# Kernel optimization log

Hardware: AMD Instinct MI355X
Metric: run time of the kernel (lower is better)

## Reference

```python
import jax, jax.numpy as jnp
import numpy as np

B, C, H, W = 16, 256, 64, 64
HEADS = 4  # kvl produces (heads-1)=3 groups: lfeat, k, v


def setup_inputs() -> dict:
    key = jax.random.key(0)
    ks = jax.random.split(key, 8)
    s = 0.02
    return {
        "x": jax.random.normal(ks[0], (B, C, H, W), jnp.float32),
        "q_input": jax.random.normal(ks[1], (B, C, H, W), jnp.float32),
        "w_kvl": jax.random.normal(ks[2], (C * (HEADS - 1), C), jnp.float32) * s,
        "b_kvl": jnp.zeros((C * (HEADS - 1),), jnp.float32),
        "w_q": jax.random.normal(ks[3], (C, C), jnp.float32) * s,
        "b_q": jnp.zeros((C,), jnp.float32),
        "w_proj": jax.random.normal(ks[4], (C, 2 * C), jnp.float32) * s,
        "b_proj": jnp.zeros((C,), jnp.float32),
    }


def gelu(x):
    return jax.nn.gelu(x, approximate=False)  # torch nn.GELU default (erf)


def reference(x, q_input, w_kvl, b_kvl, w_q, b_q, w_proj, b_proj):
    b, c, h, w = x.shape
    n = h * w
    # 1x1 conv kvl: C -> 3C, then GELU
    kvl = gelu(jnp.einsum('oc,bchw->bohw', w_kvl, x) + b_kvl[None, :, None, None])
    kvl = kvl.reshape(b, HEADS - 1, c, h, w)
    lfeat = kvl[:, 0]                      # [B,C,H,W]
    k = kvl[:, 1].reshape(b, c, n)          # [B,C,HW]
    v = kvl[:, 2].reshape(b, c, n)          # [B,C,HW]
    # 1x1 conv q: C -> C
    q = jnp.einsum('oc,bchw->bohw', w_q, q_input) + b_q[None, :, None, None]
    q = q.reshape(b, c, n)                  # [B,C,HW]
    # channel-wise attention: qk is [B,C,C] (no scaling, per source)
    qk = jnp.einsum('bcn,bdn->bcd', q, k)
    qk = jax.nn.softmax(qk, axis=-1)
    x2 = jnp.einsum('bcd,bdn->bcn', qk, v).reshape(b, c, h, w)
    cat = jnp.concatenate([lfeat, x2], axis=1)  # [B,2C,H,W]
    out = jnp.einsum('oc,bchw->bohw', w_proj, cat) + b_proj[None, :, None, None]
    return gelu(out)
```

## Files before the change

### kernel.cpp

```cpp
#include <hip/hip_runtime.h>
#include <hip/hip_bf16.h>
#include <hip/hip_fp16.h>

typedef _Float16 f16;
typedef _Float16 half8 __attribute__((ext_vector_type(8)));
typedef _Float16 half4 __attribute__((ext_vector_type(4)));
typedef float f32x4 __attribute__((ext_vector_type(4)));

__device__ __forceinline__ float gelu_f(float x) {
  return 0.5f * x * (1.0f + erff(x * 0.70710678118654752f));
}

__device__ __forceinline__ void gll16(const void* g, void* l) {
  __builtin_amdgcn_global_load_lds((const __attribute__((address_space(1))) void*)g,
                                   (__attribute__((address_space(3))) void*)l,
                                   16, 0, 0);
}

template<int KK, bool OUT_F16>
__global__ __launch_bounds__(512, 2)
void gemm_wstat(const f16* __restrict__ W, size_t sW,
                const f16* __restrict__ Act, size_t sA,
                void* __restrict__ Dv, size_t sD,
                const float* __restrict__ bias,
                int panelsPerBlock, int blocksPerBatch)
{
  constexpr int PN  = (KK == 512) ? 32 : 64;
  constexpr int PB  = PN * KK * 2;
  constexpr int NKS = KK / 32;
  constexpr int NT  = PN / 16;
  __shared__ __align__(16) char lds[2 * PB];

  const int t = threadIdx.x;
  const int l = t & 63;
  const int w = t >> 6;
  const int bid = blockIdx.x;
  const int b = bid / blocksPerBatch;
  const int blkInB = bid - b * blocksPerBatch;

  const f16* Wb = W + (size_t)b * sW;
  const f16* Ab = Act + (size_t)b * sA;

  half8 wf[2][NKS];
#pragma unroll
  for (int mt = 0; mt < 2; ++mt)
#pragma unroll
    for (int ks = 0; ks < NKS; ++ks) {
      const int row = w * 32 + mt * 16 + (l & 15);
      wf[mt][ks] = *(const half8*)(Wb + (size_t)row * KK + ks * 32 + (l >> 4) * 8);
    }

  auto stage = [&](int buf, int p) {
    const int n0 = (blkInB * panelsPerBlock + p) * PN;
#pragma unroll
    for (int i = 0; i < 4; ++i) {
      const int off = (i * 8 + w) * 1024 + l * 16;
      const int row = off / (KK * 2);
      const int chunk = (off & (KK * 2 - 1)) >> 4;
      const int lch = chunk ^ (row & 7);
      gll16(Ab + (size_t)(n0 + row) * KK + lch * 8, lds + buf * PB + (i * 8 + w) * 1024);
    }
  };

  int buf = 0;
  stage(0, 0);
  for (int p = 0; p < panelsPerBlock; ++p) {
    if (p + 1 < panelsPerBlock) {
      stage(buf ^ 1, p + 1);
      asm volatile("s_waitcnt vmcnt(4)" ::: "memory");
    } else {
      asm volatile("s_waitcnt vmcnt(0)" ::: "memory");
    }
    asm volatile("s_barrier" ::: "memory");

    f32x4 acc[2][NT];
#pragma unroll
    for (int mt = 0; mt < 2; ++mt)
#pragma unroll
      for (int nt = 0; nt < NT; ++nt)
        acc[mt][nt] = (f32x4){0.f, 0.f, 0.f, 0.f};
#pragma unroll
    for (int ks = 0; ks < NKS; ++ks) {
      half8 bf[NT];
#pragma unroll
      for (int nt = 0; nt < NT; ++nt) {
        const int row = nt * 16 + (l & 15);
        const int ch = (ks * 4 + (l >> 4)) ^ (row & 7);
        bf[nt] = *(const half8*)(lds + buf * PB + row * (KK * 2) + ch * 16);
      }
#pragma unroll
      for (int mt = 0; mt < 2; ++mt)
#pragma unroll
        for (int nt = 0; nt < NT; ++nt)
          acc[mt][nt] = __builtin_amdgcn_mfma_f32_16x16x32_f16(wf[mt][ks], bf[nt], acc[mt][nt], 0, 0, 0);
    }

    const int n0 = (blkInB * panelsPerBlock + p) * PN;
#pragma unroll
    for (int mt = 0; mt < 2; ++mt) {
      const int rb = w * 32 + mt * 16 + ((l >> 4) << 2);
#pragma unroll
      for (int nt = 0; nt < NT; ++nt) {
        const int col = n0 + nt * 16 + (l & 15);
#pragma unroll
        for (int j = 0; j < 4; ++j) {
          const int rr = rb + j;
          float v = gelu_f(acc[mt][nt][j] + bias[rr]);
          if (OUT_F16) ((f16*)Dv + (size_t)b * sD)[(size_t)rr * 4096 + col] = (f16)v;
          else         ((float*)Dv + (size_t)b * sD)[(size_t)rr * 4096 + col] = v;
        }
      }
    }
    asm volatile("s_barrier" ::: "memory");
    buf ^= 1;
  }
}

__global__ __launch_bounds__(512, 2)
void gemm_sstat(const f16* __restrict__ Act, size_t sA,
                const f16* __restrict__ W,
                f16* __restrict__ Dp, size_t sD,
                const float* __restrict__ bias,
                int panelsPerBlock, int blocksPerBatch)
{
  constexpr int KK = 256, PN = 64, PB = PN * KK * 2;
  __shared__ __align__(16) char lds[2 * PB];

  const int t = threadIdx.x;
  const int l = t & 63;
  const int w = t >> 6;
  const int bid = blockIdx.x;
  const int b = bid / blocksPerBatch;
  const int blkInB = bid - b * blocksPerBatch;

  const f16* Ab = Act + (size_t)b * sA;

  half8 wf[4][8];
#pragma unroll
  for (int ct = 0; ct < 4; ++ct)
#pragma unroll
    for (int ks = 0; ks < 8; ++ks) {
      const int row = w * 64 + ct * 16 + (l & 15);
      wf[ct][ks] = *(const half8*)(W + (size_t)row * 256 + ks * 32 + (l >> 4) * 8);
    }

  auto stage = [&](int buf, int p) {
    const int n0 = (blkInB * panelsPerBlock + p) * PN;
#pragma unroll
    for (int i = 0; i < 4; ++i) {
      const int off = (i * 8 + w) * 1024 + l * 16;
      const int row = off >> 9;
      const int chunk = (off & 511) >> 4;
      const int lch = chunk ^ (row & 7);
      gll16(Ab + (size_t)(n0 + row) * 256 + lch * 8, lds + buf * PB + (i * 8 + w) * 1024);
    }
  };

  int buf = 0;
  stage(0, 0);
  for (int p = 0; p < panelsPerBlock; ++p) {
    if (p + 1 < panelsPerBlock) {
      stage(buf ^ 1, p + 1);
      asm volatile("s_waitcnt vmcnt(4)" ::: "memory");
    } else {
      asm volatile("s_waitcnt vmcnt(0)" ::: "memory");
    }
    asm volatile("s_barrier" ::: "memory");

    f32x4 acc[4][4];
#pragma unroll
    for (int nt = 0; nt < 4; ++nt)
#pragma unroll
      for (int ct = 0; ct < 4; ++ct)
        acc[nt][ct] = (f32x4){0.f, 0.f, 0.f, 0.f};
#pragma unroll
    for (int ks = 0; ks < 8; ++ks) {
      half8 af[4];
#pragma unroll
      for (int nt = 0; nt < 4; ++nt) {
        const int row = nt * 16 + (l & 15);
        const int ch = (ks * 4 + (l >> 4)) ^ (row & 7);
        af[nt] = *(const half8*)(lds + buf * PB + row * 512 + ch * 16);
      }
#pragma unroll
      for (int nt = 0; nt < 4; ++nt)
#pragma unroll
        for (int ct = 0; ct < 4; ++ct)
          acc[nt][ct] = __builtin_amdgcn_mfma_f32_16x16x32_f16(af[nt], wf[ct][ks], acc[nt][ct], 0, 0, 0);
    }

    const int n0 = (blkInB * panelsPerBlock + p) * PN;
    f16* Db = Dp + (size_t)b * sD;
#pragma unroll
    for (int nt = 0; nt < 4; ++nt) {
      const int rb = n0 + nt * 16 + ((l >> 4) << 2);
#pragma unroll
      for (int ct = 0; ct < 4; ++ct) {
        const int col = w * 64 + ct * 16 + (l & 15);
        const int bi = col + (col >= 256 ? 256 : 0);
        const float bv = bias[bi];
#pragma unroll
        for (int j = 0; j < 4; ++j)
          Db[(size_t)(rb + j) * 512 + col] = (f16)gelu_f(acc[nt][ct][j] + bv);
      }
    }
    asm volatile("s_barrier" ::: "memory");
    buf ^= 1;
  }
}

#define BM 128
#define BN 128
#define BK 32
template<int BIAS, bool GELU_ACT, bool OUT_F16, bool KSPLIT>
__global__ __launch_bounds__(256)
void gemm_tn(const f16* __restrict__ P, size_t sP, int ldP,
             const f16* __restrict__ Q, size_t sQ, int ldQ,
             void* __restrict__ Dv, size_t sD, int ldD,
             const float* __restrict__ bias, const float* __restrict__ bias2,
             int M, int N, int K, int nks)
{
  __shared__ __align__(16) f16 ldsA[BM * BK];
  __shared__ __align__(16) f16 ldsB[BM * BK];

  const int t = threadIdx.x;
  const int l = t & 63;
  const int wid = t >> 6;
  const int wr = wid >> 1;
  const int wc = wid & 1;

  const int z = blockIdx.z;
  const int b = z / nks;
  const int s = z - b * nks;
  const int kLen = K / nks;
  const int k0 = s * kLen;

  const int mBase = blockIdx.y * BM;
  const int nBase = blockIdx.x * BN;

  const f16* Pb = P + (size_t)b * sP;
  const f16* Qb = Q + (size_t)b * sQ;

  f32x4 acc[4][4];
#pragma unroll
  for (int i = 0; i < 4; ++i)
#pragma unroll
    for (int j = 0; j < 4; ++j)
      acc[i][j] = (f32x4){0.f, 0.f, 0.f, 0.f};

  const int nk = kLen / BK;
  for (int kt = 0; kt < nk; ++kt) {
    const int kk = k0 + kt * BK;
#pragma unroll
    for (int c = 0; c < 2; ++c) {
      const int off = c * 4096 + wid * 1024 + l * 16;
      const int row = off >> 6;
      const int gch = ((off >> 4) & 3) ^ ((row >> 1) & 3);
      gll16(Pb + (size_t)(mBase + row) * ldP + kk + gch * 8,
            (char*)ldsA + c * 4096 + wid * 1024);
      gll16(Qb + (size_t)(nBase + row) * ldQ + kk + gch * 8,
            (char*)ldsB + c * 4096 + wid * 1024);
    }
    asm volatile("s_waitcnt vmcnt(0)" ::: "memory");
    __syncthreads();

    half8 af[4], bf[4];
#pragma unroll
    for (int mi = 0; mi < 4; ++mi) {
      const int row = wr * 64 + mi * 16 + (l & 15);
      const int phys = row * 64 + ((((l >> 4) ^ (row >> 1)) & 3) << 4);
      af[mi] = *(const half8*)((const char*)ldsA + phys);
    }
#pragma unroll
    for (int ni = 0; ni < 4; ++ni) {
      const int row = wc * 64 + ni * 16 + (l & 15);
      const int phys = row * 64 + ((((l >> 4) ^ (row >> 1)) & 3) << 4);
      bf[ni] = *(const half8*)((const char*)ldsB + phys);
    }
#pragma unroll
    for (int mi = 0; mi < 4; ++mi)
#pragma unroll
      for (int ni = 0; ni < 4; ++ni)
        acc[mi][ni] = __builtin_amdgcn_mfma_f32_16x16x32_f16(af[mi], bf[ni], acc[mi][ni], 0, 0, 0);
    __syncthreads();
  }

  float* Dsplit = nullptr; f16* D16 = nullptr; float* D32 = nullptr;
  if (KSPLIT)       Dsplit = (float*)Dv + (size_t)z * (size_t)(M * N);
  else if (OUT_F16) D16    = (f16*)Dv + (size_t)b * sD;
  else              D32    = (float*)Dv + (size_t)b * sD;

#pragma unroll
  for (int mi = 0; mi < 4; ++mi) {
    const int rb = mBase + wr * 64 + mi * 16 + ((l >> 4) << 2);
#pragma unroll
    for (int ni = 0; ni < 4; ++ni) {
      const int col = nBase + wc * 64 + ni * 16 + (l & 15);
#pragma unroll
      for (int j = 0; j < 4; ++j) {
        float v = acc[mi][ni][j];
        const int rr = rb + j;
        if (BIAS == 1) v += bias[rr];
        if (BIAS == 2) v += bias[col];
        if (BIAS == 3) v += bias[rr] * bias2[(size_t)b * N + col];
        if (GELU_ACT) v = gelu_f(v);
        if (KSPLIT)       Dsplit[(size_t)rr * ldD + col] = v;
        else if (OUT_F16) D16[(size_t)rr * ldD + col] = (f16)v;
        else              D32[(size_t)rr * ldD + col] = v;
      }
    }
  }
}

__global__ __launch_bounds__(256)
void transpose64(const float* __restrict__ in, f16* __restrict__ outp) {
  __shared__ float tile[64][65];
  const int b = blockIdx.z, c0 = blockIdx.y * 64, n0 = blockIdx.x * 64;
  const int t = threadIdx.x;
  const float* ib = in + (size_t)b * 1048576;
  f16* ob = outp + (size_t)b * 1048576;
  const int cl = t >> 4, c4 = t & 15;
#pragma unroll
  for (int i = 0; i < 4; ++i) {
    float4 v = *(const float4*)(ib + (size_t)(c0 + cl + i * 16) * 4096 + n0 + c4 * 4);
    tile[cl + i * 16][c4 * 4 + 0] = v.x;
    tile[cl + i * 16][c4 * 4 + 1] = v.y;
    tile[cl + i * 16][c4 * 4 + 2] = v.z;
    tile[cl + i * 16][c4 * 4 + 3] = v.w;
  }
  __syncthreads();
  const int nl = t >> 3, ch = t & 7;
#pragma unroll
  for (int i = 0; i < 2; ++i) {
    const int n = nl + i * 32;
    half8 h;
#pragma unroll
    for (int e = 0; e < 8; ++e) h[e] = (f16)tile[ch * 8 + e][n];
    *(half8*)(ob + (size_t)(n0 + n) * 256 + c0 + ch * 8) = h;
  }
}

__global__ __launch_bounds__(256)
void cvtf16(const float* __restrict__ in, f16* __restrict__ outp, int n8) {
  int i = blockIdx.x * 256 + threadIdx.x;
  if (i < n8) {
    float4 a = ((const float4*)in)[2 * i];
    float4 c = ((const float4*)in)[2 * i + 1];
    half8 h = {(f16)a.x, (f16)a.y, (f16)a.z, (f16)a.w,
               (f16)c.x, (f16)c.y, (f16)c.z, (f16)c.w};
    ((half8*)outp)[i] = h;
  }
}

__global__ __launch_bounds__(256)
void wsplit(const float* __restrict__ wp, f16* __restrict__ Wx, f16* __restrict__ Wcat) {
  const int o = blockIdx.x, c = threadIdx.x;
  const f16 lf = (f16)wp[o * 512 + c];
  Wx[o * 256 + c] = (f16)wp[o * 512 + 256 + c];
#pragma unroll
  for (int b = 0; b < 16; ++b) Wcat[(size_t)b * 131072 + o * 512 + c] = lf;
}

__global__ __launch_bounds__(256)
void ksum_k(const f16* __restrict__ kH, float* __restrict__ ks) {
  const int r = blockIdx.x * 4 + (threadIdx.x >> 6);
  const int l = threadIdx.x & 63;
  const half8* row = (const half8*)(kH + (size_t)r * 4096);
  float s = 0.f;
#pragma unroll
  for (int j = 0; j < 8; ++j) {
    half8 h = row[l + 64 * j];
#pragma unroll
    for (int e = 0; e < 8; ++e) s += (float)h[e];
  }
#pragma unroll
  for (int off = 32; off; off >>= 1) s += __shfl_xor(s, off);
  if (l == 0) ks[r] = s;
}

__global__ __launch_bounds__(256)
void reduce8_k(const float* __restrict__ part, f16* __restrict__ m1T) {
  const int i = blockIdx.x * 256 + threadIdx.x;
  const int b = i >> 14;
  const int e4 = i & 16383;
  const float4* base = (const float4*)part + (size_t)b * 131072 + e4;
  float4 s = {0.f, 0.f, 0.f, 0.f};
#pragma unroll
  for (int zz = 0; zz < 8; ++zz) {
    float4 p = base[(size_t)zz * 16384];
    s.x += p.x; s.y += p.y; s.z += p.z; s.w += p.w;
  }
  half4 h = {(f16)s.x, (f16)s.y, (f16)s.z, (f16)s.w};
  ((half4*)m1T)[i] = h;
}

__global__ __launch_bounds__(256)
void softmaxT(const float* __restrict__ qk, f16* __restrict__ pT) {
  __shared__ f16 sm[4][256];
  const int wid = threadIdx.x >> 6, l = threadIdx.x & 63;
  const int b = blockIdx.y;
  const int c = blockIdx.x * 4 + wid;
  const float* row = qk + ((size_t)b * 256 + c) * 256;
  float v[4];
#pragma unroll
  for (int j = 0; j < 4; ++j) v[j] = row[l + 64 * j];
  float m = fmaxf(fmaxf(v[0], v[1]), fmaxf(v[2], v[3]));
#pragma unroll
  for (int off = 32; off; off >>= 1) m = fmaxf(m, __shfl_xor(m, off));
  float e[4], sum = 0.f;
#pragma unroll
  for (int j = 0; j < 4; ++j) { e[j] = expf(v[j] - m); sum += e[j]; }
#pragma unroll
  for (int off = 32; off; off >>= 1) sum += __shfl_xor(sum, off);
  const float inv = 1.0f / sum;
#pragma unroll
  for (int j = 0; j < 4; ++j) sm[wid][l + 64 * j] = (f16)(e[j] * inv);
  __syncthreads();
  const int d = threadIdx.x;
  half4 h = {sm[0][d], sm[1][d], sm[2][d], sm[3][d]};
  *(half4*)(pT + ((size_t)b * 256 + d) * 256 + blockIdx.x * 4) = h;
}

extern "C" void kernel_launch(void* const* d_in, const int* in_sizes, int n_in,
                              void* d_out, int out_size, void* d_ws, size_t ws_size,
                              hipStream_t stream) {
  const float* x      = (const float*)d_in[0];
  const float* qin    = (const float*)d_in[1];
  const float* w_kvl  = (const float*)d_in[2];
  const float* b_kvl  = (const float*)d_in[3];
  const float* w_q    = (const float*)d_in[4];
  const float* b_q    = (const float*)d_in[5];
  const float* w_proj = (const float*)d_in[6];
  const float* b_proj = (const float*)d_in[7];
  float* out = (float*)d_out;
  char* ws = (char*)d_ws;

  if (ws_size < 182000000) return;

  f16*   xt    = (f16*)(ws + 0);
  float* part  = (float*)(ws + 0);
  f16*   qin16 = (f16*)(ws + 33554432);
  f16*   kH    = (f16*)(ws + 67108864);
  f16*   lvT   = (f16*)(ws + 100663296);
  f16*   wk_lv = (f16*)(ws + 167772160);
  f16*   wkK   = (f16*)(ws + 168034304);
  f16*   wq16  = (f16*)(ws + 168165376);
  f16*   Wx16  = (f16*)(ws + 168296448);
  f16*   Wcat  = (f16*)(ws + 168427520);
  float* ksum  = (float*)(ws + 172621824);
  f16*   m1T   = (f16*)(ws + 172638208);
  float* qkb   = (float*)(ws + 174735360);
  f16*   pT    = (f16*)(ws + 178929664);

  const size_t sAct = 1048576;
  dim3 blk(256), blk512(512);

  transpose64<<<dim3(64, 4, 16), blk, 0, stream>>>(x, xt);
  cvtf16<<<dim3(8192), blk, 0, stream>>>(qin, qin16, 2097152);
  cvtf16<<<dim3(32), blk, 0, stream>>>(w_kvl, wk_lv, 8192);
  cvtf16<<<dim3(32), blk, 0, stream>>>(w_kvl + 131072, wk_lv + 65536, 8192);
  cvtf16<<<dim3(32), blk, 0, stream>>>(w_kvl + 65536, wkK, 8192);
  cvtf16<<<dim3(32), blk, 0, stream>>>(w_q, wq16, 8192);
  wsplit<<<dim3(256), blk, 0, stream>>>(w_proj, Wx16, Wcat);

  hipLaunchKernelGGL((gemm_wstat<256, true>), dim3(512), blk512, 0, stream,
      wkK, (size_t)0, xt, sAct, (void*)kH, sAct, b_kvl + 256, 2, 32);
  gemm_sstat<<<dim3(512), blk512, 0, stream>>>(xt, sAct, wk_lv, lvT, (size_t)2097152, b_kvl, 2, 32);

  ksum_k<<<dim3(1024), blk, 0, stream>>>(kH, ksum);

  hipLaunchKernelGGL((gemm_tn<0, false, false, true>), dim3(2, 2, 128), blk, 0, stream,
      kH, sAct, 4096, qin16, sAct, 4096,
      (void*)part, (size_t)0, 256, (const float*)nullptr, (const float*)nullptr, 256, 256, 4096, 8);
  reduce8_k<<<dim3(1024), blk, 0, stream>>>(part, m1T);

  hipLaunchKernelGGL((gemm_tn<3, false, false, false>), dim3(2, 2, 16), blk, 0, stream,
      wq16, (size_t)0, 256, m1T, (size_t)65536, 256,
      (void*)qkb, (size_t)65536, 256, b_q, ksum, 256, 256, 256, 1);

  softmaxT<<<dim3(64, 16), blk, 0, stream>>>(qkb, pT);

  hipLaunchKernelGGL((gemm_tn<0, false, true, false>), dim3(2, 2, 16), blk, 0, stream,
      Wx16, (size_t)0, 256, pT, (size_t)65536, 256,
      (void*)(Wcat + 256), (size_t)131072, 512, (const float*)nullptr, (const float*)nullptr, 256, 256, 256, 1);

  hipLaunchKernelGGL((gemm_wstat<512, false>), dim3(512), blk512, 0, stream,
      Wcat, (size_t)131072, lvT, (size_t)2097152, (void*)out, sAct, b_proj, 4, 32);
}
```

Measured before the change: 383.9 us.

## Stage GEMM epilogues through LDS for coalesced stores; double-buffer gemm_tn loads

The weight-stationary and activation-stationary GEMMs now write their GELU outputs into the just-consumed LDS panel with a swizzled layout, then read them back as 16-byte vectors for coalesced global stores, replacing scattered 2- or 4-byte stores. Bias loads in gemm_sstat move out of the panel loop. The wait counts are adjusted for the extra outstanding stores. gemm_tn gains a double-buffered LDS prefetch with precomputed source pointers, so the next K tile loads while the current one computes. This adds barriers and LDS traffic per panel and is sensitive to whether the vmcnt values correctly count the pending loads and stores.

```diff
diff --git a/kernel.cpp b/kernel.cpp
--- a/kernel.cpp
+++ b/kernel.cpp
@@ -67,7 +67,8 @@
   for (int p = 0; p < panelsPerBlock; ++p) {
     if (p + 1 < panelsPerBlock) {
       stage(buf ^ 1, p + 1);
-      asm volatile("s_waitcnt vmcnt(4)" ::: "memory");
+      if (p == 0) asm volatile("s_waitcnt vmcnt(4)" ::: "memory");
+      else        asm volatile("s_waitcnt vmcnt(8)" ::: "memory");
     } else {
       asm volatile("s_waitcnt vmcnt(0)" ::: "memory");
     }
@@ -94,21 +95,43 @@
         for (int nt = 0; nt < NT; ++nt)
           acc[mt][nt] = __builtin_amdgcn_mfma_f32_16x16x32_f16(wf[mt][ks], bf[nt], acc[mt][nt], 0, 0, 0);
     }
+    asm volatile("s_barrier" ::: "memory");
 
     const int n0 = (blkInB * panelsPerBlock + p) * PN;
 #pragma unroll
     for (int mt = 0; mt < 2; ++mt) {
-      const int rb = w * 32 + mt * 16 + ((l >> 4) << 2);
+      const int mbase = w * 32 + mt * 16 + ((l >> 4) << 2);
 #pragma unroll
       for (int nt = 0; nt < NT; ++nt) {
-        const int col = n0 + nt * 16 + (l & 15);
+        const int ncol = nt * 16 + (l & 15);
 #pragma unroll
         for (int j = 0; j < 4; ++j) {
-          const int rr = rb + j;
-          float v = gelu_f(acc[mt][nt][j] + bias[rr]);
-          if (OUT_F16) ((f16*)Dv + (size_t)b * sD)[(size_t)rr * 4096 + col] = (f16)v;
-          else         ((float*)Dv + (size_t)b * sD)[(size_t)rr * 4096 + col] = v;
+          const int mrow = mbase + j;
+          float v = gelu_f(acc[mt][nt][j] + bias[mrow]);
+          if (OUT_F16) {
+            const int phys = mrow * 128 + ((ncol * 2) ^ ((mrow & 7) << 4));
+            *(f16*)(lds + buf * PB + phys) = (f16)v;
+          } else {
+            const int phys = mrow * 128 + ((ncol * 4) ^ ((mrow & 7) << 4));
+            *(float*)(lds + buf * PB + phys) = v;
+          }
         }
+      }
+    }
+    asm volatile("s_waitcnt lgkmcnt(0)" ::: "memory");
+    asm volatile("s_barrier" ::: "memory");
+#pragma unroll
+    for (int st = 0; st < 4; ++st) {
+      const int i = st * 8192 + t * 16;
+      const int mrow = i >> 7;
+      const int cb = i & 127;
+      const int phys = mrow * 128 + (cb ^ ((mrow & 7) << 4));
+      if (OUT_F16) {
+        half8 hv = *(const half8*)(lds + buf * PB + phys);
+        *(half8*)((char*)Dv + ((size_t)b * sD + (size_t)mrow * 4096 + n0) * 2 + cb) = hv;
+      } else {
+        float4 fv = *(const float4*)(lds + buf * PB + phys);
+        *(float4*)((char*)Dv + ((size_t)b * sD + (size_t)mrow * 4096 + n0) * 4 + cb) = fv;
       }
     }
     asm volatile("s_barrier" ::: "memory");
@@ -134,6 +157,7 @@
   const int blkInB = bid - b * blocksPerBatch;
 
   const f16* Ab = Act + (size_t)b * sA;
+  f16* Db = Dp + (size_t)b * sD;
 
   half8 wf[4][8];
 #pragma unroll
@@ -143,6 +167,13 @@
       const int row = w * 64 + ct * 16 + (l & 15);
       wf[ct][ks] = *(const half8*)(W + (size_t)row * 256 + ks * 32 + (l >> 4) * 8);
     }
+
+  float bv[4];
+#pragma unroll
+  for (int ct = 0; ct < 4; ++ct) {
+    const int col = w * 64 + ct * 16 + (l & 15);
+    bv[ct] = bias[col + (col >= 256 ? 256 : 0)];
+  }
 
   auto stage = [&](int buf, int p) {
     const int n0 = (blkInB * panelsPerBlock + p) * PN;
@@ -188,23 +219,39 @@
         for (int ct = 0; ct < 4; ++ct)
           acc[nt][ct] = __builtin_amdgcn_mfma_f32_16x16x32_f16(af[nt], wf[ct][ks], acc[nt][ct], 0, 0, 0);
     }
+    asm volatile("s_barrier" ::: "memory");
 
     const int n0 = (blkInB * panelsPerBlock + p) * PN;
-    f16* Db = Dp + (size_t)b * sD;
-#pragma unroll
-    for (int nt = 0; nt < 4; ++nt) {
-      const int rb = n0 + nt * 16 + ((l >> 4) << 2);
-#pragma unroll
-      for (int ct = 0; ct < 4; ++ct) {
-        const int col = w * 64 + ct * 16 + (l & 15);
-        const int bi = col + (col >= 256 ? 256 : 0);
-        const float bv = bias[bi];
-#pragma unroll
-        for (int j = 0; j < 4; ++j)
-          Db[(size_t)(rb + j) * 512 + col] = (f16)gelu_f(acc[nt][ct][j] + bv);
-      }
-    }
-    asm volatile("s_barrier" ::: "memory");
+#pragma unroll
+    for (int h = 0; h < 2; ++h) {
+#pragma unroll
+      for (int nt2 = 0; nt2 < 2; ++nt2) {
+        const int nt = h * 2 + nt2;
+        const int rbase = nt2 * 16 + ((l >> 4) << 2);
+#pragma unroll
+        for (int ct = 0; ct < 4; ++ct) {
+          const int colb = (w * 64 + ct * 16 + (l & 15)) * 2;
+#pragma unroll
+          for (int j = 0; j < 4; ++j) {
+            const int row = rbase + j;
+            const int phys = row * 1024 + (colb ^ (((row >> 2) & 3) << 5));
+            *(f16*)(lds + buf * PB + phys) = (f16)gelu_f(acc[nt][ct][j] + bv[ct]);
+          }
+        }
+      }
+      asm volatile("s_waitcnt lgkmcnt(0)" ::: "memory");
+      asm volatile("s_barrier" ::: "memory");
+#pragma unroll
+      for (int st = 0; st < 4; ++st) {
+        const int i = st * 8192 + t * 16;
+        const int row = i >> 10;
+        const int cb = i & 1023;
+        const int phys = row * 1024 + (cb ^ (((row >> 2) & 3) << 5));
+        half8 hv = *(const half8*)(lds + buf * PB + phys);
+        *(half8*)((char*)Db + ((size_t)(n0 + h * 32 + row) * 512) * 2 + cb) = hv;
+      }
+      asm volatile("s_barrier" ::: "memory");
+    }
     buf ^= 1;
   }
 }
@@ -220,8 +267,7 @@
              const float* __restrict__ bias, const float* __restrict__ bias2,
              int M, int N, int K, int nks)
 {
-  __shared__ __align__(16) f16 ldsA[BM * BK];
-  __shared__ __align__(16) f16 ldsB[BM * BK];
+  __shared__ __align__(16) char lds[32768];
 
   const int t = threadIdx.x;
   const int l = t & 63;
@@ -241,6 +287,29 @@
   const f16* Pb = P + (size_t)b * sP;
   const f16* Qb = Q + (size_t)b * sQ;
 
+  const f16* srcA[2];
+  const f16* srcB[2];
+  int dstOff[2];
+#pragma unroll
+  for (int c = 0; c < 2; ++c) {
+    const int off = c * 4096 + wid * 1024 + l * 16;
+    const int row = off >> 6;
+    const int gch = ((off >> 4) & 3) ^ ((row >> 1) & 3);
+    srcA[c] = Pb + (size_t)(mBase + row) * ldP + k0 + gch * 8;
+    srcB[c] = Qb + (size_t)(nBase + row) * ldQ + k0 + gch * 8;
+    dstOff[c] = c * 4096 + wid * 1024;
+  }
+
+  auto stage = [&](int bufi) {
+#pragma unroll
+    for (int c = 0; c < 2; ++c) {
+      gll16(srcA[c], lds + bufi * 8192 + dstOff[c]);
+      gll16(srcB[c], lds + 16384 + bufi * 8192 + dstOff[c]);
+      srcA[c] += BK;
+      srcB[c] += BK;
+    }
+  };
+
   f32x4 acc[4][4];
 #pragma unroll
   for (int i = 0; i < 4; ++i)
@@ -249,40 +318,37 @@
       acc[i][j] = (f32x4){0.f, 0.f, 0.f, 0.f};
 
   const int nk = kLen / BK;
+  stage(0);
+  int buf = 0;
   for (int kt = 0; kt < nk; ++kt) {
-    const int kk = k0 + kt * BK;
-#pragma unroll
-    for (int c = 0; c < 2; ++c) {
-      const int off = c * 4096 + wid * 1024 + l * 16;
-      const int row = off >> 6;
-      const int gch = ((off >> 4) & 3) ^ ((row >> 1) & 3);
-      gll16(Pb + (size_t)(mBase + row) * ldP + kk + gch * 8,
-            (char*)ldsA + c * 4096 + wid * 1024);
-      gll16(Qb + (size_t)(nBase + row) * ldQ + kk + gch * 8,
-            (char*)ldsB + c * 4096 + wid * 1024);
-    }
-    asm volatile("s_waitcnt vmcnt(0)" ::: "memory");
-    __syncthreads();
+    if (kt + 1 < nk) {
+      stage(buf ^ 1);
+      asm volatile("s_waitcnt vmcnt(4)" ::: "memory");
+    } else {
+      asm volatile("s_waitcnt vmcnt(0)" ::: "memory");
+    }
+    asm volatile("s_barrier" ::: "memory");
 
     half8 af[4], bf[4];
 #pragma unroll
     for (int mi = 0; mi < 4; ++mi) {
       const int row = wr * 64 + mi * 16 + (l & 15);
       const int phys = row * 64 + ((((l >> 4) ^ (row >> 1)) & 3) << 4);
-      af[mi] = *(const half8*)((const char*)ldsA + phys);
+      af[mi] = *(const half8*)(lds + buf * 8192 + phys);
     }
 #pragma unroll
     for (int ni = 0; ni < 4; ++ni) {
       const int row = wc * 64 + ni * 16 + (l & 15);
       const int phys = row * 64 + ((((l >> 4) ^ (row >> 1)) & 3) << 4);
-      bf[ni] = *(const half8*)((const char*)ldsB + phys);
+      bf[ni] = *(const half8*)(lds + 16384 + buf * 8192 + phys);
     }
 #pragma unroll
     for (int mi = 0; mi < 4; ++mi)
 #pragma unroll
       for (int ni = 0; ni < 4; ++ni)
         acc[mi][ni] = __builtin_amdgcn_mfma_f32_16x16x32_f16(af[mi], bf[ni], acc[mi][ni], 0, 0, 0);
-    __syncthreads();
+    asm volatile("s_barrier" ::: "memory");
+    buf ^= 1;
   }
 
   float* Dsplit = nullptr; f16* D16 = nullptr; float* D32 = nullptr;
```

After: 389.7 us. No clear change (+1.5%).
